# Optimization experiments

Measured on AMD Instinct MI355X. Metric: run time of the kernel, lower is better.

The kernel has to match this reference:

```python
import jax, jax.numpy as jnp
import numpy as np

B, N, E, D = 2, 4096, 1024, 128  # batch, seq, embed_dim, expand_ratio (head dim)
H = E // D                        # 8 heads
LN_EPS = 1e-5


def setup_inputs() -> dict:
    key = jax.random.key(0)
    ks = jax.random.split(key, 6)
    s = 0.02
    return {
        "x": jax.random.normal(ks[0], (B, N, E), jnp.float32),
        "W_in": jax.random.normal(ks[1], (3 * E, E), jnp.float32) * s,
        "W_out": jax.random.normal(ks[2], (E, E), jnp.float32) * s,
        "W_g1": jax.random.normal(ks[3], (D, E), jnp.float32) * s,
        "W_g2": jax.random.normal(ks[4], (E, D), jnp.float32) * s,
        "ln_w": jnp.ones((E,), jnp.float32),
    }


def _gla_scan(q, k, v, g):
    # q,k,v,g: [b,h,n,d]; GLA recurrence: S_t = exp(g_t)[:,None]*S_{t-1} + k_t v_t^T; o_t = q_t @ S_t
    def step(S, inp):
        qt, kt, vt, gt = inp  # each [b,h,d]
        S = jnp.exp(gt)[..., None] * S + kt[..., None] * vt[..., None, :]  # [b,h,d,d]
        ot = jnp.einsum('bhd,bhde->bhe', qt, S)
        return S, ot

    xs = tuple(jnp.moveaxis(a, 2, 0) for a in (q, k, v, g))  # [n,b,h,d]
    S0 = jnp.zeros(q.shape[:2] + (q.shape[-1], v.shape[-1]), q.dtype)
    _, o = jax.lax.scan(step, S0, xs)
    return jnp.moveaxis(o, 0, 2)  # [b,h,n,d]


def reference(x, W_in, W_out, W_g1, W_g2, ln_w):
    b, n, e = x.shape
    u = x @ W_in.T                       # [b,n,3E]
    v, q, lg = jnp.split(u, 3, axis=-1)  # note order: v, q, log_f
    q = jax.nn.silu(q)                   # q_activation = silu
    f = jax.nn.sigmoid(lg)
    k = 1.0 - f                          # non_sparse_ratio == 1 path
    g = jax.nn.log_sigmoid(lg)           # log of forget gate

    def tohead(a):
        return a.reshape(b, n, H, D).transpose(0, 2, 1, 3)  # b h n d

    o = _gla_scan(tohead(q), tohead(k), tohead(v), tohead(g))
    o = o.transpose(0, 2, 1, 3).reshape(b, n, e)  # b n (h d)

    gate = jax.nn.sigmoid((x @ W_g1.T) @ W_g2.T)  # low-rank output gate
    o = o * gate

    mu = jnp.mean(o, axis=-1, keepdims=True)
    var = jnp.var(o, axis=-1, keepdims=True)
    o = (o - mu) * jax.lax.rsqrt(var + LN_EPS) * ln_w  # layernorm, no bias
    return o @ W_out.T
```

## Files before the change

kernel.cpp:

```cpp
#include <hip/hip_runtime.h>
#include <cmath>

#define B_ 2
#define N_ 4096
#define E_ 1024
#define D_ 128
#define H_ 8
#define CHUNK 64
#define NC_ (N_/CHUNK)

__device__ __forceinline__ float sigmoidf_(float x){ return 1.f/(1.f + __expf(-x)); }

__device__ __forceinline__ unsigned short f2bf(float f){
    unsigned u = __float_as_uint(f);
    u += 0x7FFFu + ((u >> 16) & 1u);
    return (unsigned short)(u >> 16);
}
__device__ __forceinline__ float bf2f(unsigned short s){
    return __uint_as_float(((unsigned)s) << 16);
}
__device__ __forceinline__ unsigned short f2bf_fast(float f){
    __bf16 h = (__bf16)f;
    return __builtin_bit_cast(unsigned short, h);
}

typedef __attribute__((ext_vector_type(8))) __bf16 bf16x8;
typedef __attribute__((ext_vector_type(4))) float  f32x4;
typedef __attribute__((address_space(3))) unsigned int as3_u32;
typedef __attribute__((address_space(1))) unsigned int as1_u32;

__device__ __forceinline__ void gload_lds16(const void* g, void* l){
    __builtin_amdgcn_global_load_lds((as1_u32*)g, (as3_u32*)l, 16, 0, 0);
}

__device__ __forceinline__ bf16x8 ldsfrag256(const unsigned short* Lp, int row, int kg){
    return *reinterpret_cast<const bf16x8*>(&Lp[row*128 + ((kg ^ (row&7))<<3)]);
}
__device__ __forceinline__ bf16x8 ldsfrag128(const unsigned short* Lp, int row, int kg){
    return *reinterpret_cast<const bf16x8*>(&Lp[row*64 + ((kg ^ (row&7))<<3)]);
}

template<bool OUT_BF16>
__global__ __launch_bounds__(256) void gemm_bf16(
    const unsigned short* __restrict__ A,
    const unsigned short* __restrict__ Bw,
    void* __restrict__ Cout, int M, int N, int K)
{
    __shared__ unsigned short As[128*64];
    __shared__ unsigned short Bs[128*64];
    const int tid  = threadIdx.x;
    const int wave = tid >> 6;
    const int lane = tid & 63;
    const int gx = gridDim.x;
    const int nwg = gx * gridDim.y;
    int bid = blockIdx.y*gx + blockIdx.x;
    bid = (bid & 7)*(nwg >> 3) + (bid >> 3);
    const int m0 = (bid / gx) * 128, n0 = (bid % gx) * 128;
    const int wr = (wave >> 1) * 64;
    const int wc = (wave & 1) * 64;
    const int l15 = lane & 15, l4 = lane >> 4;
    const int p = l15 & 7;

    f32x4 acc[4][4];
#pragma unroll
    for (int i=0;i<4;i++)
#pragma unroll
        for (int j=0;j<4;j++)
#pragma unroll
            for (int q=0;q<4;q++) acc[i][j][q]=0.f;

    const int srow = wave*32 + (lane>>3);
    const int sgrp = lane & 7;

    for (int k0=0; k0<K; k0+=64){
        if (k0) __syncthreads();
#pragma unroll
        for (int i=0;i<4;i++){
            const int r  = srow + 8*i;
            const int cg = sgrp ^ (r & 7);
            gload_lds16(A  + (size_t)(m0 + r)*K + k0 + cg*8, &As[(wave*32 + 8*i)*64]);
            gload_lds16(Bw + (size_t)(n0 + r)*K + k0 + cg*8, &Bs[(wave*32 + 8*i)*64]);
        }
        __syncthreads();
#pragma unroll
        for (int ks=0; ks<2; ks++){
            bf16x8 av[4], bv[4];
            const int tA = (((ks<<2) | l4) ^ p) << 3;
#pragma unroll
            for (int f=0; f<4; f++){
                const int rowA = wr + f*16 + l15;
                const int rowB = wc + f*16 + l15;
                av[f] = *reinterpret_cast<const bf16x8*>(&As[(rowA<<6) + tA]);
                bv[f] = *reinterpret_cast<const bf16x8*>(&Bs[(rowB<<6) + tA]);
            }
#pragma unroll
            for (int fm=0; fm<4; fm++)
#pragma unroll
                for (int fn=0; fn<4; fn++)
                    acc[fm][fn] = __builtin_amdgcn_mfma_f32_16x16x32_bf16(
                        av[fm], bv[fn], acc[fm][fn], 0, 0, 0);
        }
    }
    const int crow0 = m0 + wr + l4*4;
    const int ccol0 = n0 + wc + l15;
    if (!OUT_BF16){
        float* C = (float*)Cout;
#pragma unroll
        for (int fm=0; fm<4; fm++)
#pragma unroll
            for (int fn=0; fn<4; fn++)
#pragma unroll
                for (int j=0;j<4;j++)
                    C[(size_t)(crow0 + fm*16 + j)*N + ccol0 + fn*16] = acc[fm][fn][j];
    } else {
        unsigned short* C = (unsigned short*)Cout;
#pragma unroll
        for (int fm=0; fm<4; fm++)
#pragma unroll
            for (int fn=0; fn<4; fn++)
#pragma unroll
                for (int j=0;j<4;j++)
                    C[(size_t)(crow0 + fm*16 + j)*N + ccol0 + fn*16] = f2bf(acc[fm][fn][j]);
    }
}

__global__ __launch_bounds__(256) void cast_bf16(
    const float* __restrict__ in, unsigned short* __restrict__ out, int n4)
{
    for (int i = blockIdx.x*256 + threadIdx.x; i < n4; i += gridDim.x*256){
        const float4 v = reinterpret_cast<const float4*>(in)[i];
        ushort4 o;
        o.x = f2bf(v.x); o.y = f2bf(v.y); o.z = f2bf(v.z); o.w = f2bf(v.w);
        reinterpret_cast<ushort4*>(out)[i] = o;
    }
}

__global__ __launch_bounds__(512) void gla_prep(
    const unsigned short* __restrict__ u, float* __restrict__ EBC,
    unsigned short* __restrict__ QSb, unsigned short* __restrict__ KINb,
    unsigned short* __restrict__ KINtb, unsigned short* __restrict__ Vtb)
{
    __shared__ float tot[4*128];
    const int bid = blockIdx.x;
    const int c  = bid % NC_;
    const int hh = (bid / NC_) % H_;
    const int b  = bid / (NC_*H_);
    const int d  = threadIdx.x & 127;
    const int qd = threadIdx.x >> 7;
    const int t0 = qd*16;
    const size_t urow0 = ((size_t)b*N_ + (size_t)c*CHUNK)*(3*E_) + (size_t)hh*D_ + d;

    float bl[16], qv[16], vv[16];
#pragma unroll
    for (int i=0;i<16;i++)
        bl[i] = bf2f(u[urow0 + (size_t)(t0+i)*(3*E_) + 2*E_]);
#pragma unroll
    for (int i=0;i<16;i++)
        qv[i] = bf2f(u[urow0 + (size_t)(t0+i)*(3*E_) + E_]);
#pragma unroll
    for (int i=0;i<16;i++)
        vv[i] = bf2f(u[urow0 + (size_t)(t0+i)*(3*E_)]);

    float acc = 0.f;
#pragma unroll
    for (int i=0;i<16;i++){
        const float lg = bl[i];
        const float e  = __expf(-fabsf(lg));
        const float g  = fminf(lg, 0.f) - __logf(1.f + e);
        acc += g;
        bl[i] = acc;
    }
    tot[qd*128 + d] = acc;
    __syncthreads();
    const float s0 = tot[d], s1 = tot[128+d], s2 = tot[256+d], s3 = tot[384+d];
    const float off = (qd>0 ? s0 : 0.f) + (qd>1 ? s1 : 0.f) + (qd>2 ? s2 : 0.f);
    const float bcv = s0 + s1 + s2 + s3;
    const float ebc = __expf(bcv);
    if (threadIdx.x < 128) EBC[(size_t)bid*D_ + d] = ebc;

    unsigned kin_pk[8], v_pk[8];
    float prev = 0.f;
    const size_t obase = (size_t)bid*CHUNK*D_;
#pragma unroll
    for (int i=0;i<16;i++){
        const int t = t0 + i;
        const float Bl = bl[i];
        const float g  = Bl - prev;  prev = Bl;
        const float Bc = Bl + off;
        const float kk = 1.f - __expf(g);
        const float eB = __expf(Bc);
        const float q  = qv[i];
        const float es = __expf(-q);
        const float silu = q * __builtin_amdgcn_rcpf(1.f + es);
        const float qs  = silu * eB;
        const float kin = kk * __builtin_amdgcn_rcpf(eB);
        QSb [obase + (size_t)t*D_ + d] = f2bf_fast(qs);
        KINb[obase + (size_t)t*D_ + d] = f2bf_fast(kin);
        const unsigned kb = f2bf_fast(kin * ebc);
        const unsigned vb = f2bf_fast(vv[i]);
        if (i & 1){ kin_pk[i>>1] |= kb<<16; v_pk[i>>1] |= vb<<16; }
        else      { kin_pk[i>>1]  = kb;     v_pk[i>>1]  = vb;     }
    }
    const size_t tbase = (size_t)bid*D_*CHUNK + (size_t)d*CHUNK + t0;
#pragma unroll
    for (int j=0;j<2;j++){
        uint4 kq, vq;
        kq.x=kin_pk[4*j]; kq.y=kin_pk[4*j+1]; kq.z=kin_pk[4*j+2]; kq.w=kin_pk[4*j+3];
        vq.x=v_pk[4*j];   vq.y=v_pk[4*j+1];   vq.z=v_pk[4*j+2];   vq.w=v_pk[4*j+3];
        *reinterpret_cast<uint4*>(&KINtb[tbase + j*8]) = kq;
        *reinterpret_cast<uint4*>(&Vtb  [tbase + j*8]) = vq;
    }
}

__global__ __launch_bounds__(256) void gla_chunk_mm(
    const unsigned short* __restrict__ Vtb,
    const unsigned short* __restrict__ KINtb,
    unsigned short* __restrict__ McTb)
{
    __shared__ unsigned short As[128*64];
    __shared__ unsigned short Bs[128*64];
    const int bid = blockIdx.x;
    const int tid = threadIdx.x;
    const int w = tid >> 6, lane = tid & 63;
    const int l15 = lane & 15, l4 = lane >> 4;
    const int wr = (w >> 1) * 64, wc = (w & 1) * 64;
    const unsigned short* A  = Vtb   + (size_t)bid*128*64;
    const unsigned short* Bp = KINtb + (size_t)bid*128*64;

    f32x4 acc[4][4];
#pragma unroll
    for (int i=0;i<4;i++)
#pragma unroll
        for (int j=0;j<4;j++)
#pragma unroll
            for (int q=0;q<4;q++) acc[i][j][q]=0.f;

#pragma unroll
    for (int i=0;i<4;i++){
        const int r  = w*32 + i*8 + (lane>>3);
        const int gs = (lane&7) ^ (r&7);
        gload_lds16(A  + (size_t)r*64 + gs*8, &As[(w*32+i*8)*64]);
        gload_lds16(Bp + (size_t)r*64 + gs*8, &Bs[(w*32+i*8)*64]);
    }
    __syncthreads();
#pragma unroll
    for (int ks=0; ks<2; ks++){
        bf16x8 av[4], bv[4];
#pragma unroll
        for (int f=0; f<4; f++){
            av[f] = ldsfrag128(As, wr + f*16 + l15, ks*4 + l4);
            bv[f] = ldsfrag128(Bs, wc + f*16 + l15, ks*4 + l4);
        }
#pragma unroll
        for (int fm=0; fm<4; fm++)
#pragma unroll
            for (int fn=0; fn<4; fn++)
                acc[fm][fn] = __builtin_amdgcn_mfma_f32_16x16x32_bf16(
                    av[fm], bv[fn], acc[fm][fn], 0, 0, 0);
    }
    unsigned short* C = McTb + (size_t)bid*128*128;
#pragma unroll
    for (int fm=0; fm<4; fm++)
#pragma unroll
        for (int fn=0; fn<4; fn++)
#pragma unroll
            for (int j=0;j<4;j++)
                C[(size_t)(wr + fm*16 + l4*4 + j)*128 + wc + fn*16 + l15] = f2bf(acc[fm][fn][j]);
}

__global__ __launch_bounds__(256) void gla_scan_chunks(
    const unsigned short* __restrict__ McTb, const float* __restrict__ EBC,
    unsigned short* __restrict__ Sb16)
{
    const size_t F = (size_t)blockIdx.x*256 + threadIdx.x;
    const int bh = (int)(F >> 14);
    const int rem = (int)(F & 16383);
    const int d = rem & 127;
    float S = 0.f;
    for (int c=0;c<NC_;c++){
        const size_t idx = (((size_t)bh*NC_ + c) << 14) + rem;
        const float m = bf2f(McTb[idx]);
        const float dec = EBC[((size_t)bh*NC_ + c)*D_ + d];
        Sb16[idx] = f2bf(S);
        S = dec*S + m;
    }
}

__global__ __launch_bounds__(256) void gla_output(
    const unsigned short* __restrict__ QSb,
    const unsigned short* __restrict__ KINb,
    const unsigned short* __restrict__ Vtb,
    const unsigned short* __restrict__ Sb,
    float* __restrict__ Opre)
{
    __shared__ unsigned short QS_l[64*128];
    __shared__ unsigned short KA_l[64*128];
    __shared__ unsigned short Vt_l[128*64];
    __shared__ unsigned short S_l [128*128];
    const int bid = blockIdx.x;
    const int c = bid % NC_;
    const int h = (bid / NC_) % H_;
    const int b = bid / (NC_*H_);
    const int tid = threadIdx.x;
    const int w = tid >> 6, lane = tid & 63;
    const int l15 = lane & 15, l4 = lane >> 4;

    {
        const unsigned short* q = QSb + (size_t)bid*64*128;
        const unsigned short* k = KINb + (size_t)bid*64*128;
        const unsigned short* v = Vtb + (size_t)bid*128*64;
        const unsigned short* s = Sb  + (size_t)bid*128*128;
#pragma unroll
        for (int i=0;i<4;i++){
            const int r  = w*16 + i*4 + (lane>>4);
            const int gs = (lane&15) ^ (r&7);
            gload_lds16(q + (size_t)r*128 + gs*8, &QS_l[(w*16+i*4)*128]);
            gload_lds16(k + (size_t)r*128 + gs*8, &KA_l[(w*16+i*4)*128]);
        }
#pragma unroll
        for (int i=0;i<4;i++){
            const int r  = w*32 + i*8 + (lane>>3);
            const int gs = (lane&7) ^ (r&7);
            gload_lds16(v + (size_t)r*64 + gs*8, &Vt_l[(w*32+i*8)*64]);
        }
#pragma unroll
        for (int i=0;i<8;i++){
            const int r  = w*32 + i*4 + (lane>>4);
            const int gs = (lane&15) ^ (r&7);
            gload_lds16(s + (size_t)r*128 + gs*8, &S_l[(w*32+i*4)*128]);
        }
    }
    __syncthreads();

    f32x4 accA[4];
#pragma unroll
    for (int i=0;i<4;i++)
#pragma unroll
        for (int q=0;q<4;q++) accA[i][q]=0.f;
    const int srow = w*16 + l15;
#pragma unroll
    for (int ks=0; ks<4; ks++){
        const bf16x8 bv = ldsfrag256(KA_l, srow, ks*4 + l4);
#pragma unroll
        for (int ft=0; ft<4; ft++){
            const bf16x8 av = ldsfrag256(QS_l, ft*16 + l15, ks*4 + l4);
            accA[ft] = __builtin_amdgcn_mfma_f32_16x16x32_bf16(av, bv, accA[ft], 0,0,0);
        }
    }
    __syncthreads();
#pragma unroll
    for (int ft=0; ft<4; ft++)
#pragma unroll
        for (int j=0;j<4;j++){
            const int t = ft*16 + l4*4 + j;
            const int s = w*16 + l15;
            const float vA = (t >= s) ? accA[ft][j] : 0.f;
            KA_l[t*64 + (((s>>3) ^ (t&7))<<3) + (s&7)] = f2bf(vA);
        }
    __syncthreads();

    f32x4 acc[4][2];
#pragma unroll
    for (int i=0;i<4;i++)
#pragma unroll
        for (int j=0;j<2;j++)
#pragma unroll
            for (int q=0;q<4;q++) acc[i][j][q]=0.f;
#pragma unroll
    for (int ks=0; ks<2; ks++){
        bf16x8 bv[2];
        bv[0] = ldsfrag128(Vt_l, w*32 +      l15, ks*4 + l4);
        bv[1] = ldsfrag128(Vt_l, w*32 + 16 + l15, ks*4 + l4);
#pragma unroll
        for (int ft=0; ft<4; ft++){
            const bf16x8 av = ldsfrag128(KA_l, ft*16 + l15, ks*4 + l4);
            acc[ft][0] = __builtin_amdgcn_mfma_f32_16x16x32_bf16(av, bv[0], acc[ft][0], 0,0,0);
            acc[ft][1] = __builtin_amdgcn_mfma_f32_16x16x32_bf16(av, bv[1], acc[ft][1], 0,0,0);
        }
    }
#pragma unroll
    for (int ks=0; ks<4; ks++){
        bf16x8 bv[2];
        bv[0] = ldsfrag256(S_l, w*32 +      l15, ks*4 + l4);
        bv[1] = ldsfrag256(S_l, w*32 + 16 + l15, ks*4 + l4);
#pragma unroll
        for (int ft=0; ft<4; ft++){
            const bf16x8 av = ldsfrag256(QS_l, ft*16 + l15, ks*4 + l4);
            acc[ft][0] = __builtin_amdgcn_mfma_f32_16x16x32_bf16(av, bv[0], acc[ft][0], 0,0,0);
            acc[ft][1] = __builtin_amdgcn_mfma_f32_16x16x32_bf16(av, bv[1], acc[ft][1], 0,0,0);
        }
    }
    const size_t rowbase = (size_t)b*N_ + (size_t)c*CHUNK;
#pragma unroll
    for (int ft=0; ft<4; ft++)
#pragma unroll
        for (int fe=0; fe<2; fe++)
#pragma unroll
            for (int j=0;j<4;j++){
                const int t = ft*16 + l4*4 + j;
                const int e = w*32 + fe*16 + l15;
                Opre[(rowbase + t)*E_ + h*D_ + e] = acc[ft][fe][j];
            }
}

__global__ __launch_bounds__(256) void gate_ln_bf16(
    const float* __restrict__ O, const unsigned short* __restrict__ G2,
    const float* __restrict__ lnw, unsigned short* __restrict__ Ob)
{
    const int row = blockIdx.x;
    const int tid = threadIdx.x;
    const size_t off = (size_t)row*E_ + tid*4;
    float4 o = *reinterpret_cast<const float4*>(&O[off]);
    const ushort4 gu = *reinterpret_cast<const ushort4*>(&G2[off]);
    o.x *= sigmoidf_(bf2f(gu.x)); o.y *= sigmoidf_(bf2f(gu.y));
    o.z *= sigmoidf_(bf2f(gu.z)); o.w *= sigmoidf_(bf2f(gu.w));
    float s1 = o.x+o.y+o.z+o.w;
    float s2 = o.x*o.x + o.y*o.y + o.z*o.z + o.w*o.w;
#pragma unroll
    for (int sh=32; sh>0; sh>>=1){
        s1 += __shfl_down(s1, sh);
        s2 += __shfl_down(s2, sh);
    }
    __shared__ float r1[4], r2[4];
    const int wid = tid >> 6;
    if ((tid & 63)==0){ r1[wid]=s1; r2[wid]=s2; }
    __syncthreads();
    s1 = r1[0]+r1[1]+r1[2]+r1[3];
    s2 = r2[0]+r2[1]+r2[2]+r2[3];
    const float mean = s1 * (1.f/E_);
    const float var  = s2 * (1.f/E_) - mean*mean;
    const float rs   = rsqrtf(var + 1e-5f);
    const float4 w = *reinterpret_cast<const float4*>(&lnw[tid*4]);
    ushort4 r;
    r.x = f2bf((o.x-mean)*rs*w.x); r.y = f2bf((o.y-mean)*rs*w.y);
    r.z = f2bf((o.z-mean)*rs*w.z); r.w = f2bf((o.w-mean)*rs*w.w);
    *reinterpret_cast<ushort4*>(&Ob[off]) = r;
}

extern "C" void kernel_launch(void* const* d_in, const int* in_sizes, int n_in,
                              void* d_out, int out_size, void* d_ws, size_t ws_size,
                              hipStream_t stream)
{
    const float* x     = (const float*)d_in[0];
    const float* W_in  = (const float*)d_in[1];
    const float* W_out = (const float*)d_in[2];
    const float* W_g1  = (const float*)d_in[3];
    const float* W_g2  = (const float*)d_in[4];
    const float* lnw   = (const float*)d_in[5];
    float* out = (float*)d_out;
    char* ws = (char*)d_ws;

    unsigned short* ub     = (unsigned short*)(ws);
    unsigned short* McTb   = (unsigned short*)(ws);
    unsigned short* Sb16   = (unsigned short*)(ws + 33554432);
    float*          EBC    = (float*)(ws + 100663296);
    unsigned short* QSb    = (unsigned short*)(ws + 101187584);
    unsigned short* KINb   = (unsigned short*)(ws + 117964800);
    unsigned short* KINtb  = (unsigned short*)(ws + 134742016);
    unsigned short* Vtb    = (unsigned short*)(ws + 151519232);
    float*          Opre   = (float*)(ws + 168296448);
    unsigned short* xb     = (unsigned short*)(ws + 201850880);
    unsigned short* W_inb  = (unsigned short*)(ws + 218628096);
    unsigned short* W_outb = (unsigned short*)(ws + 224919552);
    unsigned short* W_g1b  = (unsigned short*)(ws + 227016704);
    unsigned short* W_g2b  = (unsigned short*)(ws + 227278848);
    unsigned short* G1b    = (unsigned short*)(ws + 227540992);
    unsigned short* ObF    = (unsigned short*)(ws + 229638144);
    unsigned short* G2b    = QSb;

    const int M = B_*N_;
    dim3 blk(256);

    cast_bf16<<<2048, blk, 0, stream>>>(x,     xb,     (B_*N_*E_)/4);
    cast_bf16<<<2048, blk, 0, stream>>>(W_in,  W_inb,  (3*E_*E_)/4);
    cast_bf16<<<1024, blk, 0, stream>>>(W_out, W_outb, (E_*E_)/4);
    cast_bf16<<<128,  blk, 0, stream>>>(W_g1,  W_g1b,  (D_*E_)/4);
    cast_bf16<<<128,  blk, 0, stream>>>(W_g2,  W_g2b,  (E_*D_)/4);

    gemm_bf16<true><<<dim3(3*E_/128, M/128), blk, 0, stream>>>(xb, W_inb, ub, M, 3*E_, E_);
    gla_prep<<<dim3(B_*H_*NC_), dim3(512), 0, stream>>>(ub, EBC, QSb, KINb, KINtb, Vtb);
    gla_chunk_mm<<<dim3(B_*H_*NC_), blk, 0, stream>>>(Vtb, KINtb, McTb);
    gla_scan_chunks<<<dim3((B_*H_*D_*D_)/256), blk, 0, stream>>>(McTb, EBC, Sb16);
    gla_output<<<dim3(B_*H_*NC_), blk, 0, stream>>>(QSb, KINb, Vtb, Sb16, Opre);
    gemm_bf16<true><<<dim3(1, M/128), blk, 0, stream>>>(xb, W_g1b, G1b, M, D_, E_);
    gemm_bf16<true><<<dim3(E_/128, M/128), blk, 0, stream>>>(G1b, W_g2b, G2b, M, E_, D_);
    gate_ln_bf16<<<dim3(M), blk, 0, stream>>>(Opre, G2b, lnw, ObF);
    gemm_bf16<false><<<dim3(E_/128, M/128), blk, 0, stream>>>(ObF, W_outb, out, M, E_, E_);
}
```

Measured before the change: 215.0 us.

## Add double-buffered 256x256 GEMM kernel and fuse bf16 cast launches

Introduces a 512-thread GEMM with 256x256 tiles, double-buffered LDS, and register-staged prefetch of the next K-tile interleaved with MFMA work. It is used for the input projection and the output projection. The five separate fp32-to-bf16 cast launches are merged into one kernel that walks all buffers in a single grid. The larger tiles raise arithmetic intensity and cut launch overhead, but they use more LDS and registers and give fewer workgroups (for example 4x32 for the output GEMM), which may underfill the GPU.

Result: slower. 350.8 us (+63.2%).

```diff
diff --git a/kernel.cpp b/kernel.cpp
--- a/kernel.cpp
+++ b/kernel.cpp
@@ -38,6 +38,112 @@
 }
 __device__ __forceinline__ bf16x8 ldsfrag128(const unsigned short* Lp, int row, int kg){
     return *reinterpret_cast<const bf16x8*>(&Lp[row*64 + ((kg ^ (row&7))<<3)]);
+}
+
+template<bool OUT_BF16>
+__global__ __launch_bounds__(512) void gemm256(
+    const unsigned short* __restrict__ Ag,
+    const unsigned short* __restrict__ Bg,
+    void* __restrict__ Cout, int M, int N, int K)
+{
+    __shared__ unsigned short As_[2][256*64];
+    __shared__ unsigned short Bs_[2][256*64];
+    const int tid  = threadIdx.x;
+    const int wave = tid >> 6;
+    const int lane = tid & 63;
+    const int l15 = lane & 15, l4 = lane >> 4;
+    const int wm = wave >> 2, wn = wave & 3;
+
+    const int gx = gridDim.x;
+    const int nwg = gx * gridDim.y;
+    int bid = blockIdx.y*gx + blockIdx.x;
+    bid = (bid & 7)*(nwg >> 3) + (bid >> 3);
+    const int m0 = (bid / gx) * 256, n0 = (bid % gx) * 256;
+
+    f32x4 acc[8][4];
+#pragma unroll
+    for (int i=0;i<8;i++)
+#pragma unroll
+        for (int j=0;j<4;j++)
+#pragma unroll
+            for (int q=0;q<4;q++) acc[i][j][q]=0.f;
+
+    bf16x8 a[4][2], b[2][2];
+    uint4 s0a[4], s0b[4], s1a[4], s1b[4];
+
+#pragma unroll
+    for (int j=0;j<4;j++){
+        const int rbase = wave*32 + j*8;
+        const int row = rbase + (lane>>3);
+        const int grp = (lane&7) ^ (row&7);
+        gload_lds16(Ag + (size_t)(m0+row)*K + grp*8, &As_[0][rbase*64]);
+        gload_lds16(Bg + (size_t)(n0+row)*K + grp*8, &Bs_[0][rbase*64]);
+    }
+    __syncthreads();
+
+#define ISSUE_A(RS, KO) { _Pragma("unroll") \
+    for (int i_=0;i_<4;i_++){ const int idx_=i_*512+tid, r_=idx_>>3, g_=idx_&7; \
+        RS[i_] = *reinterpret_cast<const uint4*>(Ag + (size_t)(m0+r_)*K + (KO) + g_*8); } }
+#define ISSUE_B(RS, KO) { _Pragma("unroll") \
+    for (int i_=0;i_<4;i_++){ const int idx_=i_*512+tid, r_=idx_>>3, g_=idx_&7; \
+        RS[i_] = *reinterpret_cast<const uint4*>(Bg + (size_t)(n0+r_)*K + (KO) + g_*8); } }
+#define WRITE_S(RS, DST) { _Pragma("unroll") \
+    for (int i_=0;i_<4;i_++){ const int idx_=i_*512+tid, r_=idx_>>3, g_=idx_&7; \
+        *reinterpret_cast<uint4*>(&DST[r_*64 + ((g_ ^ (r_&7))<<3)]) = RS[i_]; } }
+#define RD_A(SRC, MQ) { _Pragma("unroll") for (int f_=0;f_<4;f_++) _Pragma("unroll") \
+    for (int k_=0;k_<2;k_++) a[f_][k_] = ldsfrag128(SRC, wm*128 + (MQ)*64 + f_*16 + l15, k_*4 + l4); }
+#define RD_B(SRC, NQ) { _Pragma("unroll") for (int f_=0;f_<2;f_++) _Pragma("unroll") \
+    for (int k_=0;k_<2;k_++) b[f_][k_] = ldsfrag128(SRC, wn*64 + (NQ)*32 + f_*16 + l15, k_*4 + l4); }
+#define MM(MQ, NQ) { __builtin_amdgcn_s_setprio(1); _Pragma("unroll") \
+    for (int f_=0;f_<4;f_++) _Pragma("unroll") for (int f2_=0;f2_<2;f2_++) _Pragma("unroll") \
+    for (int k_=0;k_<2;k_++) acc[(MQ)*4+f_][(NQ)*2+f2_] = __builtin_amdgcn_mfma_f32_16x16x32_bf16( \
+        a[f_][k_], b[f2_][k_], acc[(MQ)*4+f_][(NQ)*2+f2_], 0,0,0); __builtin_amdgcn_s_setprio(0); }
+#define KITER(CUR, RSWa, RSWb, RSIa, RSIb, KNEXT) { \
+    const unsigned short* Ac = As_[CUR]; const unsigned short* Bc = Bs_[CUR]; \
+    unsigned short* An = As_[1-(CUR)]; unsigned short* Bn = Bs_[1-(CUR)]; \
+    RD_A(Ac, 0); RD_B(Bc, 0); ISSUE_A(RSIa, KNEXT); MM(0,0); \
+    RD_B(Bc, 1); ISSUE_B(RSIb, KNEXT); MM(0,1); \
+    RD_A(Ac, 1); WRITE_S(RSWa, An); MM(1,1); \
+    RD_B(Bc, 0); WRITE_S(RSWb, Bn); MM(1,0); \
+    __syncthreads(); }
+
+    const int NT = K >> 6;
+    ISSUE_A(s0a, 64); ISSUE_B(s0b, 64);
+    for (int U = 0; U < NT; U += 2){
+        const int kn1 = (U+2 < NT) ? (U+2)*64 : 0;
+        const int kn2 = (U+3 < NT) ? (U+3)*64 : 0;
+        KITER(0, s0a, s0b, s1a, s1b, kn1);
+        KITER(1, s1a, s1b, s0a, s0b, kn2);
+    }
+#undef ISSUE_A
+#undef ISSUE_B
+#undef WRITE_S
+#undef RD_A
+#undef RD_B
+#undef MM
+#undef KITER
+
+    const int crow0 = m0 + wm*128 + l4*4;
+    const int ccol0 = n0 + wn*64 + l15;
+    if (!OUT_BF16){
+        float* C = (float*)Cout;
+#pragma unroll
+        for (int fm=0; fm<8; fm++)
+#pragma unroll
+            for (int fn=0; fn<4; fn++)
+#pragma unroll
+                for (int j=0;j<4;j++)
+                    C[(size_t)(crow0 + fm*16 + j)*N + ccol0 + fn*16] = acc[fm][fn][j];
+    } else {
+        unsigned short* C = (unsigned short*)Cout;
+#pragma unroll
+        for (int fm=0; fm<8; fm++)
+#pragma unroll
+            for (int fn=0; fn<4; fn++)
+#pragma unroll
+                for (int j=0;j<4;j++)
+                    C[(size_t)(crow0 + fm*16 + j)*N + ccol0 + fn*16] = f2bf(acc[fm][fn][j]);
+    }
 }
 
 template<bool OUT_BF16>
@@ -124,14 +230,31 @@
     }
 }
 
-__global__ __launch_bounds__(256) void cast_bf16(
-    const float* __restrict__ in, unsigned short* __restrict__ out, int n4)
-{
-    for (int i = blockIdx.x*256 + threadIdx.x; i < n4; i += gridDim.x*256){
-        const float4 v = reinterpret_cast<const float4*>(in)[i];
+#define CQ0 2097152
+#define CQ1 786432
+#define CQ2 262144
+#define CQ3 32768
+#define CQ4 32768
+__global__ __launch_bounds__(256) void cast_all(
+    const float* __restrict__ x,  const float* __restrict__ w1,
+    const float* __restrict__ w2, const float* __restrict__ w3,
+    const float* __restrict__ w4,
+    unsigned short* __restrict__ xb,  unsigned short* __restrict__ w1b,
+    unsigned short* __restrict__ w2b, unsigned short* __restrict__ w3b,
+    unsigned short* __restrict__ w4b)
+{
+    const int total = CQ0+CQ1+CQ2+CQ3+CQ4;
+    for (int i = blockIdx.x*256 + threadIdx.x; i < total; i += gridDim.x*256){
+        const float* src; unsigned short* dst; int off;
+        if (i < CQ0){ src=x; dst=xb; off=i; }
+        else if (i < CQ0+CQ1){ src=w1; dst=w1b; off=i-CQ0; }
+        else if (i < CQ0+CQ1+CQ2){ src=w2; dst=w2b; off=i-CQ0-CQ1; }
+        else if (i < CQ0+CQ1+CQ2+CQ3){ src=w3; dst=w3b; off=i-CQ0-CQ1-CQ2; }
+        else { src=w4; dst=w4b; off=i-CQ0-CQ1-CQ2-CQ3; }
+        const float4 v = reinterpret_cast<const float4*>(src)[off];
         ushort4 o;
         o.x = f2bf(v.x); o.y = f2bf(v.y); o.z = f2bf(v.z); o.w = f2bf(v.w);
-        reinterpret_cast<ushort4*>(out)[i] = o;
+        reinterpret_cast<ushort4*>(dst)[off] = o;
     }
 }
 
@@ -471,13 +594,10 @@
     const int M = B_*N_;
     dim3 blk(256);
 
-    cast_bf16<<<2048, blk, 0, stream>>>(x,     xb,     (B_*N_*E_)/4);
-    cast_bf16<<<2048, blk, 0, stream>>>(W_in,  W_inb,  (3*E_*E_)/4);
-    cast_bf16<<<1024, blk, 0, stream>>>(W_out, W_outb, (E_*E_)/4);
-    cast_bf16<<<128,  blk, 0, stream>>>(W_g1,  W_g1b,  (D_*E_)/4);
-    cast_bf16<<<128,  blk, 0, stream>>>(W_g2,  W_g2b,  (E_*D_)/4);
-
-    gemm_bf16<true><<<dim3(3*E_/128, M/128), blk, 0, stream>>>(xb, W_inb, ub, M, 3*E_, E_);
+    cast_all<<<2048, blk, 0, stream>>>(x, W_in, W_out, W_g1, W_g2,
+                                       xb, W_inb, W_outb, W_g1b, W_g2b);
+
+    gemm256<true><<<dim3(3*E_/256, M/256), dim3(512), 0, stream>>>(xb, W_inb, ub, M, 3*E_, E_);
     gla_prep<<<dim3(B_*H_*NC_), dim3(512), 0, stream>>>(ub, EBC, QSb, KINb, KINtb, Vtb);
     gla_chunk_mm<<<dim3(B_*H_*NC_), blk, 0, stream>>>(Vtb, KINtb, McTb);
     gla_scan_chunks<<<dim3((B_*H_*D_*D_)/256), blk, 0, stream>>>(McTb, EBC, Sb16);
@@ -485,5 +605,5 @@
     gemm_bf16<true><<<dim3(1, M/128), blk, 0, stream>>>(xb, W_g1b, G1b, M, D_, E_);
     gemm_bf16<true><<<dim3(E_/128, M/128), blk, 0, stream>>>(G1b, W_g2b, G2b, M, E_, D_);
     gate_ln_bf16<<<dim3(M), blk, 0, stream>>>(Opre, G2b, lnw, ObF);
-    gemm_bf16<false><<<dim3(E_/128, M/128), blk, 0, stream>>>(ObF, W_outb, out, M, E_, E_);
-}
+    gemm256<false><<<dim3(E_/256, M/256), dim3(512), 0, stream>>>(ObF, W_outb, out, M, E_, E_);
+}
```

## Fuse gate into GLA output, load operands to registers, merge cast kernels

Applied to the files above, without the earlier changes.

Merges the five fp32-to-bf16 cast launches into one kernel. In gla_output, the K, V^T and S operands are loaded straight from global memory into registers instead of through LDS, which cuts LDS use and one barrier. The sigmoid output gate is folded into gla_output, which now writes bf16 instead of fp32, so the layernorm kernel reads half the bytes and does no gate work. G2 moves to its own workspace region and its GEMMs run before gla_output; the extra rounding of O to bf16 before layernorm could slightly affect accuracy.

After: 202.7 us. 1.06x faster.

```diff
diff --git a/kernel.cpp b/kernel.cpp
--- a/kernel.cpp
+++ b/kernel.cpp
@@ -38,6 +38,9 @@
 }
 __device__ __forceinline__ bf16x8 ldsfrag128(const unsigned short* Lp, int row, int kg){
     return *reinterpret_cast<const bf16x8*>(&Lp[row*64 + ((kg ^ (row&7))<<3)]);
+}
+__device__ __forceinline__ bf16x8 u4_to_bf(uint4 u){
+    return __builtin_bit_cast(bf16x8, u);
 }
 
 template<bool OUT_BF16>
@@ -124,14 +127,31 @@
     }
 }
 
-__global__ __launch_bounds__(256) void cast_bf16(
-    const float* __restrict__ in, unsigned short* __restrict__ out, int n4)
-{
-    for (int i = blockIdx.x*256 + threadIdx.x; i < n4; i += gridDim.x*256){
-        const float4 v = reinterpret_cast<const float4*>(in)[i];
+#define CQ0 2097152
+#define CQ1 786432
+#define CQ2 262144
+#define CQ3 32768
+#define CQ4 32768
+__global__ __launch_bounds__(256) void cast_all(
+    const float* __restrict__ x,  const float* __restrict__ w1,
+    const float* __restrict__ w2, const float* __restrict__ w3,
+    const float* __restrict__ w4,
+    unsigned short* __restrict__ xb,  unsigned short* __restrict__ w1b,
+    unsigned short* __restrict__ w2b, unsigned short* __restrict__ w3b,
+    unsigned short* __restrict__ w4b)
+{
+    const int total = CQ0+CQ1+CQ2+CQ3+CQ4;
+    for (int i = blockIdx.x*256 + threadIdx.x; i < total; i += gridDim.x*256){
+        const float* src; unsigned short* dst; int off;
+        if (i < CQ0){ src=x; dst=xb; off=i; }
+        else if (i < CQ0+CQ1){ src=w1; dst=w1b; off=i-CQ0; }
+        else if (i < CQ0+CQ1+CQ2){ src=w2; dst=w2b; off=i-CQ0-CQ1; }
+        else if (i < CQ0+CQ1+CQ2+CQ3){ src=w3; dst=w3b; off=i-CQ0-CQ1-CQ2; }
+        else { src=w4; dst=w4b; off=i-CQ0-CQ1-CQ2-CQ3; }
+        const float4 v = reinterpret_cast<const float4*>(src)[off];
         ushort4 o;
         o.x = f2bf(v.x); o.y = f2bf(v.y); o.z = f2bf(v.z); o.w = f2bf(v.w);
-        reinterpret_cast<ushort4*>(out)[i] = o;
+        reinterpret_cast<ushort4*>(dst)[off] = o;
     }
 }
 
@@ -291,12 +311,11 @@
     const unsigned short* __restrict__ KINb,
     const unsigned short* __restrict__ Vtb,
     const unsigned short* __restrict__ Sb,
-    float* __restrict__ Opre)
+    const unsigned short* __restrict__ G2b,
+    unsigned short* __restrict__ Opre)
 {
     __shared__ unsigned short QS_l[64*128];
-    __shared__ unsigned short KA_l[64*128];
-    __shared__ unsigned short Vt_l[128*64];
-    __shared__ unsigned short S_l [128*128];
+    __shared__ unsigned short A_l [64*64];
     const int bid = blockIdx.x;
     const int c = bid % NC_;
     const int h = (bid / NC_) % H_;
@@ -305,49 +324,52 @@
     const int w = tid >> 6, lane = tid & 63;
     const int l15 = lane & 15, l4 = lane >> 4;
 
+    const unsigned short* qb = QSb + (size_t)bid*64*128;
+    const unsigned short* kb = KINb + (size_t)bid*64*128;
+    const unsigned short* vb = Vtb + (size_t)bid*128*64;
+    const unsigned short* sb = Sb  + (size_t)bid*128*128;
+
+#pragma unroll
+    for (int i=0;i<4;i++){
+        const int r  = w*16 + i*4 + (lane>>4);
+        const int gs = (lane&15) ^ (r&7);
+        gload_lds16(qb + (size_t)r*128 + gs*8, &QS_l[(w*16+i*4)*128]);
+    }
+    uint4 kinr[4];
     {
-        const unsigned short* q = QSb + (size_t)bid*64*128;
-        const unsigned short* k = KINb + (size_t)bid*64*128;
-        const unsigned short* v = Vtb + (size_t)bid*128*64;
-        const unsigned short* s = Sb  + (size_t)bid*128*128;
-#pragma unroll
-        for (int i=0;i<4;i++){
-            const int r  = w*16 + i*4 + (lane>>4);
-            const int gs = (lane&15) ^ (r&7);
-            gload_lds16(q + (size_t)r*128 + gs*8, &QS_l[(w*16+i*4)*128]);
-            gload_lds16(k + (size_t)r*128 + gs*8, &KA_l[(w*16+i*4)*128]);
-        }
-#pragma unroll
-        for (int i=0;i<4;i++){
-            const int r  = w*32 + i*8 + (lane>>3);
-            const int gs = (lane&7) ^ (r&7);
-            gload_lds16(v + (size_t)r*64 + gs*8, &Vt_l[(w*32+i*8)*64]);
-        }
-#pragma unroll
-        for (int i=0;i<8;i++){
-            const int r  = w*32 + i*4 + (lane>>4);
-            const int gs = (lane&15) ^ (r&7);
-            gload_lds16(s + (size_t)r*128 + gs*8, &S_l[(w*32+i*4)*128]);
-        }
+        const int srow = w*16 + l15;
+#pragma unroll
+        for (int ks=0; ks<4; ks++)
+            kinr[ks] = *reinterpret_cast<const uint4*>(kb + (size_t)srow*128 + (ks*4 + l4)*8);
     }
     __syncthreads();
 
+    uint4 vtr[2][2], sr[2][4];
+#pragma unroll
+    for (int fe=0; fe<2; fe++){
+        const int row = w*32 + fe*16 + l15;
+#pragma unroll
+        for (int ks=0; ks<2; ks++)
+            vtr[fe][ks] = *reinterpret_cast<const uint4*>(vb + (size_t)row*64 + (ks*4 + l4)*8);
+#pragma unroll
+        for (int ks=0; ks<4; ks++)
+            sr[fe][ks]  = *reinterpret_cast<const uint4*>(sb + (size_t)row*128 + (ks*4 + l4)*8);
+    }
+
     f32x4 accA[4];
 #pragma unroll
     for (int i=0;i<4;i++)
 #pragma unroll
         for (int q=0;q<4;q++) accA[i][q]=0.f;
-    const int srow = w*16 + l15;
 #pragma unroll
     for (int ks=0; ks<4; ks++){
-        const bf16x8 bv = ldsfrag256(KA_l, srow, ks*4 + l4);
+        const bf16x8 bv = u4_to_bf(kinr[ks]);
 #pragma unroll
         for (int ft=0; ft<4; ft++){
             const bf16x8 av = ldsfrag256(QS_l, ft*16 + l15, ks*4 + l4);
             accA[ft] = __builtin_amdgcn_mfma_f32_16x16x32_bf16(av, bv, accA[ft], 0,0,0);
         }
     }
-    __syncthreads();
 #pragma unroll
     for (int ft=0; ft<4; ft++)
 #pragma unroll
@@ -355,7 +377,7 @@
             const int t = ft*16 + l4*4 + j;
             const int s = w*16 + l15;
             const float vA = (t >= s) ? accA[ft][j] : 0.f;
-            KA_l[t*64 + (((s>>3) ^ (t&7))<<3) + (s&7)] = f2bf(vA);
+            A_l[t*64 + (((s>>3) ^ (t&7))<<3) + (s&7)] = f2bf(vA);
         }
     __syncthreads();
 
@@ -368,26 +390,24 @@
             for (int q=0;q<4;q++) acc[i][j][q]=0.f;
 #pragma unroll
     for (int ks=0; ks<2; ks++){
-        bf16x8 bv[2];
-        bv[0] = ldsfrag128(Vt_l, w*32 +      l15, ks*4 + l4);
-        bv[1] = ldsfrag128(Vt_l, w*32 + 16 + l15, ks*4 + l4);
+        const bf16x8 b0 = u4_to_bf(vtr[0][ks]);
+        const bf16x8 b1 = u4_to_bf(vtr[1][ks]);
 #pragma unroll
         for (int ft=0; ft<4; ft++){
-            const bf16x8 av = ldsfrag128(KA_l, ft*16 + l15, ks*4 + l4);
-            acc[ft][0] = __builtin_amdgcn_mfma_f32_16x16x32_bf16(av, bv[0], acc[ft][0], 0,0,0);
-            acc[ft][1] = __builtin_amdgcn_mfma_f32_16x16x32_bf16(av, bv[1], acc[ft][1], 0,0,0);
+            const bf16x8 av = ldsfrag128(A_l, ft*16 + l15, ks*4 + l4);
+            acc[ft][0] = __builtin_amdgcn_mfma_f32_16x16x32_bf16(av, b0, acc[ft][0], 0,0,0);
+            acc[ft][1] = __builtin_amdgcn_mfma_f32_16x16x32_bf16(av, b1, acc[ft][1], 0,0,0);
         }
     }
 #pragma unroll
     for (int ks=0; ks<4; ks++){
-        bf16x8 bv[2];
-        bv[0] = ldsfrag256(S_l, w*32 +      l15, ks*4 + l4);
-        bv[1] = ldsfrag256(S_l, w*32 + 16 + l15, ks*4 + l4);
+        const bf16x8 b0 = u4_to_bf(sr[0][ks]);
+        const bf16x8 b1 = u4_to_bf(sr[1][ks]);
 #pragma unroll
         for (int ft=0; ft<4; ft++){
             const bf16x8 av = ldsfrag256(QS_l, ft*16 + l15, ks*4 + l4);
-            acc[ft][0] = __builtin_amdgcn_mfma_f32_16x16x32_bf16(av, bv[0], acc[ft][0], 0,0,0);
-            acc[ft][1] = __builtin_amdgcn_mfma_f32_16x16x32_bf16(av, bv[1], acc[ft][1], 0,0,0);
+            acc[ft][0] = __builtin_amdgcn_mfma_f32_16x16x32_bf16(av, b0, acc[ft][0], 0,0,0);
+            acc[ft][1] = __builtin_amdgcn_mfma_f32_16x16x32_bf16(av, b1, acc[ft][1], 0,0,0);
         }
     }
     const size_t rowbase = (size_t)b*N_ + (size_t)c*CHUNK;
@@ -399,21 +419,22 @@
             for (int j=0;j<4;j++){
                 const int t = ft*16 + l4*4 + j;
                 const int e = w*32 + fe*16 + l15;
-                Opre[(rowbase + t)*E_ + h*D_ + e] = acc[ft][fe][j];
+                const size_t idx = (rowbase + t)*E_ + h*D_ + e;
+                const float g = sigmoidf_(bf2f(G2b[idx]));
+                Opre[idx] = f2bf(acc[ft][fe][j] * g);
             }
 }
 
-__global__ __launch_bounds__(256) void gate_ln_bf16(
-    const float* __restrict__ O, const unsigned short* __restrict__ G2,
-    const float* __restrict__ lnw, unsigned short* __restrict__ Ob)
+__global__ __launch_bounds__(256) void ln_bf16(
+    const unsigned short* __restrict__ O, const float* __restrict__ lnw,
+    unsigned short* __restrict__ Ob)
 {
     const int row = blockIdx.x;
     const int tid = threadIdx.x;
     const size_t off = (size_t)row*E_ + tid*4;
-    float4 o = *reinterpret_cast<const float4*>(&O[off]);
-    const ushort4 gu = *reinterpret_cast<const ushort4*>(&G2[off]);
-    o.x *= sigmoidf_(bf2f(gu.x)); o.y *= sigmoidf_(bf2f(gu.y));
-    o.z *= sigmoidf_(bf2f(gu.z)); o.w *= sigmoidf_(bf2f(gu.w));
+    const ushort4 ov = *reinterpret_cast<const ushort4*>(&O[off]);
+    float4 o;
+    o.x = bf2f(ov.x); o.y = bf2f(ov.y); o.z = bf2f(ov.z); o.w = bf2f(ov.w);
     float s1 = o.x+o.y+o.z+o.w;
     float s2 = o.x*o.x + o.y*o.y + o.z*o.z + o.w*o.w;
 #pragma unroll
@@ -453,12 +474,13 @@
     unsigned short* ub     = (unsigned short*)(ws);
     unsigned short* McTb   = (unsigned short*)(ws);
     unsigned short* Sb16   = (unsigned short*)(ws + 33554432);
+    unsigned short* G2b    = (unsigned short*)(ws + 67108864);
     float*          EBC    = (float*)(ws + 100663296);
     unsigned short* QSb    = (unsigned short*)(ws + 101187584);
     unsigned short* KINb   = (unsigned short*)(ws + 117964800);
     unsigned short* KINtb  = (unsigned short*)(ws + 134742016);
     unsigned short* Vtb    = (unsigned short*)(ws + 151519232);
-    float*          Opre   = (float*)(ws + 168296448);
+    unsigned short* Opre   = (unsigned short*)(ws + 168296448);
     unsigned short* xb     = (unsigned short*)(ws + 201850880);
     unsigned short* W_inb  = (unsigned short*)(ws + 218628096);
     unsigned short* W_outb = (unsigned short*)(ws + 224919552);
@@ -466,24 +488,20 @@
     unsigned short* W_g2b  = (unsigned short*)(ws + 227278848);
     unsigned short* G1b    = (unsigned short*)(ws + 227540992);
     unsigned short* ObF    = (unsigned short*)(ws + 229638144);
-    unsigned short* G2b    = QSb;
 
     const int M = B_*N_;
     dim3 blk(256);
 
-    cast_bf16<<<2048, blk, 0, stream>>>(x,     xb,     (B_*N_*E_)/4);
-    cast_bf16<<<2048, blk, 0, stream>>>(W_in,  W_inb,  (3*E_*E_)/4);
-    cast_bf16<<<1024, blk, 0, stream>>>(W_out, W_outb, (E_*E_)/4);
-    cast_bf16<<<128,  blk, 0, stream>>>(W_g1,  W_g1b,  (D_*E_)/4);
-    cast_bf16<<<128,  blk, 0, stream>>>(W_g2,  W_g2b,  (E_*D_)/4);
+    cast_all<<<2048, blk, 0, stream>>>(x, W_in, W_out, W_g1, W_g2,
+                                       xb, W_inb, W_outb, W_g1b, W_g2b);
 
     gemm_bf16<true><<<dim3(3*E_/128, M/128), blk, 0, stream>>>(xb, W_inb, ub, M, 3*E_, E_);
     gla_prep<<<dim3(B_*H_*NC_), dim3(512), 0, stream>>>(ub, EBC, QSb, KINb, KINtb, Vtb);
     gla_chunk_mm<<<dim3(B_*H_*NC_), blk, 0, stream>>>(Vtb, KINtb, McTb);
     gla_scan_chunks<<<dim3((B_*H_*D_*D_)/256), blk, 0, stream>>>(McTb, EBC, Sb16);
-    gla_output<<<dim3(B_*H_*NC_), blk, 0, stream>>>(QSb, KINb, Vtb, Sb16, Opre);
     gemm_bf16<true><<<dim3(1, M/128), blk, 0, stream>>>(xb, W_g1b, G1b, M, D_, E_);
     gemm_bf16<true><<<dim3(E_/128, M/128), blk, 0, stream>>>(G1b, W_g2b, G2b, M, E_, D_);
-    gate_ln_bf16<<<dim3(M), blk, 0, stream>>>(Opre, G2b, lnw, ObF);
+    gla_output<<<dim3(B_*H_*NC_), blk, 0, stream>>>(QSb, KINb, Vtb, Sb16, G2b, Opre);
+    ln_bf16<<<dim3(M), blk, 0, stream>>>(Opre, lnw, ObF);
     gemm_bf16<false><<<dim3(E_/128, M/128), blk, 0, stream>>>(ObF, W_outb, out, M, E_, E_);
 }
```
